# Kernel optimization log

Measured on AMD Instinct MI355X. Metric: run time of the kernel, lower is better.

Reference implementation:

```python
import jax, jax.numpy as jnp
import numpy as np

N = 524288      # points per view
S = 256         # superpoint segments
SEG = N // S    # points per segment (2048 >= 30 -> no small segments)
C = 96          # backbone_out_channels
K = 30          # samples per segment (matching_max_pair//S = 32 >= 30 -> capped at 30)
NEG = 30        # negatives sampled per anchor row
T_SUP = 0.5     # SupConLoss temperature
EPS = 1e-7


def setup_inputs() -> dict:
    key = jax.random.key(0)
    ks = jax.random.split(key, 4)
    view1_feat = jax.random.normal(ks[0], (N, C), jnp.float32)
    view2_feat = jax.random.normal(ks[1], (N, C), jnp.float32)
    region = (jnp.arange(N, dtype=jnp.int32) // SEG).astype(jnp.int32)
    # evenly spaced K sample indices inside each contiguous segment
    off = jnp.linspace(0.0, SEG - 1, K).astype(jnp.int32)
    idx_samples = (jnp.arange(S, dtype=jnp.int32)[:, None] * SEG + off[None, :]).reshape(-1)
    bg_mask = (jnp.arange(S) % 4) == 0  # some background superpoints
    gq_w = jax.random.normal(ks[2], (C, C), jnp.float32) * 0.02
    gk_w = jax.random.normal(ks[3], (C, C), jnp.float32) * 0.02
    z = jnp.zeros((C,), jnp.float32)
    o = jnp.ones((C,), jnp.float32)
    return dict(view1_feat=view1_feat, view2_feat=view2_feat,
                gq_w=gq_w, gq_b=z, gq_gamma=o, gq_beta=z,
                gk_w=gk_w, gk_b=z, gk_gamma=o, gk_beta=z,
                view1_region=region, view2_region=region,
                idx_samples=idx_samples, bg_mask=bg_mask)


def _head(x, w, b, gamma, beta):
    # Linear -> BatchNorm1d (batch stats, training mode) -> ReLU
    y = x @ w.T + b
    mu = y.mean(axis=0)
    var = jnp.var(y, axis=0)
    y = (y - mu) * jax.lax.rsqrt(var + 1e-5) * gamma + beta
    return jax.nn.relu(y)


def _segment_mean(x, seg, n):
    s = jax.ops.segment_sum(x, seg, num_segments=n)
    cnt = jax.ops.segment_sum(jnp.ones((x.shape[0], 1), x.dtype), seg, num_segments=n)
    return s / jnp.maximum(cnt, 1.0)


def _l2norm(x):
    return x / (jnp.linalg.norm(x, axis=1, keepdims=True) + EPS)


def _supcon(sim, pos, neg):
    # SupConLoss(temperature=0.5, scale_by_temperature=False, is_positive_in_denom=True)
    logits = sim / T_SUP
    denom_mask = pos | neg
    neg_inf = jnp.finfo(logits.dtype).min
    lse = jax.scipy.special.logsumexp(jnp.where(denom_mask, logits, neg_inf), axis=1)
    log_prob = logits - lse[:, None]
    row = jnp.sum(jnp.where(pos, log_prob, 0.0), axis=1) / jnp.sum(pos, axis=1).astype(logits.dtype)
    return -jnp.mean(row)


def reference(view1_feat, view2_feat, gq_w, gq_b, gq_gamma, gq_beta,
              gk_w, gk_b, gk_gamma, gk_beta,
              view1_region, view2_region, idx_samples, bg_mask):
    Sk = S * K
    rows = jnp.arange(S)[:, None]

    # ---- Lcon: raw-feature superpoint anchors vs sampled points ----
    anchor = _l2norm(_segment_mean(view2_feat, view2_region, S))          # [S, C]
    samples = _l2norm(view1_feat[idx_samples])                            # [S*K, C]
    sim = anchor @ samples.T                                              # [S, S*K]

    col_seg = jnp.arange(Sk) // K
    pos1 = rows == col_seg[None, :]                                       # block-diagonal positives

    # 30 evenly spaced negatives among the Sk-K non-positive columns per row
    M = Sk - K
    p = jnp.linspace(0.0, M - 1, NEG).astype(jnp.int32)                   # [NEG]
    actual = jnp.where(p[None, :] < rows * K, p[None, :], p[None, :] + K) # skip own block
    neg1 = jnp.zeros((S, Sk), bool).at[jnp.broadcast_to(rows, (S, NEG)), actual].set(True)
    Lcon = _supcon(sim, pos1, neg1)

    # ---- Lcon_2: projected (g_q / g_k head) features, top-k positives, background-split negatives ----
    v2g = _head(view2_feat, gq_w, gq_b, gq_gamma, gq_beta)
    v1g = _head(view1_feat, gk_w, gk_b, gk_gamma, gk_beta)
    anchor2 = _l2norm(_segment_mean(v2g, view2_region, S))
    samples2 = _l2norm(v1g[idx_samples])
    sim2 = anchor2 @ samples2.T                                           # [S, S*K]

    _, tk = jax.lax.top_k(sim2, K)
    pos2 = jnp.zeros((S, Sk), bool).at[jnp.broadcast_to(rows, (S, K)), tk].set(True)

    bg_col = jnp.repeat(bg_mask, K)                                       # [S*K]
    neg2 = jnp.where(bg_mask[:, None], ~bg_col[None, :], bg_col[None, :]) & (~pos1)
    Lcon2 = _supcon(sim2, pos2, neg2)

    return Lcon + Lcon2


if __name__ == '__main__':
    out = reference(**setup_inputs())
    print(out)
```

## Files before the change

### kernel.cpp

```cpp
#include <hip/hip_runtime.h>
#include <math.h>

#define SK 7680
#define NPTS 524288

#define WS_GQ_PART  0
#define WS_GK_PART  6144
#define WS_GQ_SCALE 12288
#define WS_GQ_SHIFT 12384
#define WS_GK_SCALE 12480
#define WS_GK_SHIFT 12576
#define WS_SEGX2    21888
#define WS_SEGG2    46464
#define WS_ANCHOR1  71040
#define WS_ANCHOR2  95616
#define WS_SAMPT    120192
#define WS_SAMP2T   857472
#define WS_SROW     1594752
#define WS_ZERO_CNT 71040

typedef __attribute__((ext_vector_type(8))) short bf16x8;
typedef __attribute__((ext_vector_type(4))) float f32x4;

#define AS1 __attribute__((address_space(1)))
#define AS3 __attribute__((address_space(3)))

__device__ __forceinline__ void gl16(const float* g, char* l){
  __builtin_amdgcn_global_load_lds((const AS1 unsigned*)g, (AS3 unsigned*)l, 16, 0, 0);
}

__device__ __forceinline__ bf16x8 pack8(float4 a, float4 b){
  union { unsigned u[4]; bf16x8 v; } r;
  asm("v_cvt_pk_bf16_f32 %0, %1, %2" : "=v"(r.u[0]) : "v"(a.x), "v"(a.y));
  asm("v_cvt_pk_bf16_f32 %0, %1, %2" : "=v"(r.u[1]) : "v"(a.z), "v"(a.w));
  asm("v_cvt_pk_bf16_f32 %0, %1, %2" : "=v"(r.u[2]) : "v"(b.x), "v"(b.y));
  asm("v_cvt_pk_bf16_f32 %0, %1, %2" : "=v"(r.u[3]) : "v"(b.z), "v"(b.w));
  return r.v;
}
__device__ __forceinline__ bf16x8 pack8v(f32x4 a, f32x4 b){
  union { unsigned u[4]; bf16x8 v; } r;
  asm("v_cvt_pk_bf16_f32 %0, %1, %2" : "=v"(r.u[0]) : "v"(a[0]), "v"(a[1]));
  asm("v_cvt_pk_bf16_f32 %0, %1, %2" : "=v"(r.u[1]) : "v"(a[2]), "v"(a[3]));
  asm("v_cvt_pk_bf16_f32 %0, %1, %2" : "=v"(r.u[2]) : "v"(b[0]), "v"(b[1]));
  asm("v_cvt_pk_bf16_f32 %0, %1, %2" : "=v"(r.u[3]) : "v"(b[2]), "v"(b[3]));
  return r.v;
}
__device__ __forceinline__ float4 ld4(const float* p){
  return *reinterpret_cast<const float4*>(p);
}

__device__ __forceinline__ void build_wf(const float* __restrict__ W, bf16x8 wf[3][3],
                                         int oh, int lr, int g){
  #pragma unroll
  for (int i=0;i<3;i++){
    const float* wr = W + (unsigned)((oh*3+i)*16+lr)*96 + g*8;
    #pragma unroll
    for (int kt=0;kt<3;kt++)
      wf[i][kt] = pack8(ld4(wr + kt*32), ld4(wr + kt*32 + 4));
  }
}

#define VMC_WAIT(it)                                                   \
  if ((it) <= 4)      { asm volatile("s_waitcnt vmcnt(9)" ::: "memory"); } \
  else if ((it) == 5) { asm volatile("s_waitcnt vmcnt(6)" ::: "memory"); } \
  else if ((it) == 6) { asm volatile("s_waitcnt vmcnt(3)" ::: "memory"); } \
  else                { asm volatile("s_waitcnt vmcnt(0)" ::: "memory"); }

__global__ __launch_bounds__(256) void stats_both(
    const float* __restrict__ V1, const float* __restrict__ V2,
    const float* __restrict__ Wk, const float* __restrict__ Wq,
    float* __restrict__ gpartK, float* __restrict__ gpartQ)
{
  __shared__ __align__(16) float xtile[4][3072];
  __shared__ float red[96];
  __shared__ float red2[96];
  const int tid = threadIdx.x;
  const int l = tid & 63, w = tid >> 6;
  const int g = l >> 4, lr = l & 15;
  const int rg = w & 1, oh = w >> 1;
  const int R = rg*16 + lr;

  const int r_ = blockIdx.x & 15;
  const int g_ = blockIdx.x >> 4;
  const bool isv2 = (r_ >= 8);
  const int  sub  = (r_ & 7) * 256 + g_;
  const float* X = isv2 ? V2 : V1;
  const float* W = isv2 ? Wq : Wk;

  bf16x8 wf[3][3];
  build_wf(W, wf, oh, lr, g);
  if (tid < 96){ red[tid]=0.f; red2[tid]=0.f; }

  int so[3];
  #pragma unroll
  for (int i=0;i<3;i++){
    int s = i*256 + tid;
    int r = s/24, cp = s%24;
    int c = (cp & ~7) | ((cp & 7) ^ (r & 7));
    so[i] = r*96 + c*4;
  }
  const float* base = X + (long)sub*24576;
  char* lbase_c = (char*)&xtile[0][0] + w*1024;

  unsigned lb = (unsigned)(uintptr_t)&xtile[0][0];
  const unsigned a0base = lb + R*384 + (unsigned)((( 2*g   ) ^ (R&7))*16);
  const unsigned a1base = lb + R*384 + (unsigned)((((2*g)|1) ^ (R&7))*16);

#define STAGE(t) {                                        \
    const float* tb = base + (t)*3072;                    \
    char* ld = lbase_c + ((t)&3)*12288;                   \
    gl16(tb + so[0], ld);                                 \
    gl16(tb + so[1], ld + 4096);                          \
    gl16(tb + so[2], ld + 8192); }

  STAGE(0) STAGE(1) STAGE(2) STAGE(3)

  float sY[3]={0.f,0.f,0.f}, sY2[3]={0.f,0.f,0.f};

  #pragma unroll 1
  for (int it=0; it<8; ++it){
    VMC_WAIT(it)
    __builtin_amdgcn_s_barrier();
    const unsigned boff = (unsigned)(it&3)*12288u;
    unsigned addrA = a0base + boff, addrB = a1base + boff;
    f32x4 xA0,xA1,xA2,xB0,xB1,xB2;
    asm volatile(
      "ds_read_b128 %0, %6\n\t"
      "ds_read_b128 %1, %6 offset:128\n\t"
      "ds_read_b128 %2, %6 offset:256\n\t"
      "ds_read_b128 %3, %7\n\t"
      "ds_read_b128 %4, %7 offset:128\n\t"
      "ds_read_b128 %5, %7 offset:256\n\t"
      "s_waitcnt lgkmcnt(0)"
      : "=&v"(xA0),"=&v"(xA1),"=&v"(xA2),"=&v"(xB0),"=&v"(xB1),"=&v"(xB2)
      : "v"(addrA), "v"(addrB) : "memory");
    __builtin_amdgcn_sched_barrier(0);
    __builtin_amdgcn_s_barrier();
    if (it<4) STAGE(it+4)
    bf16x8 a0 = pack8v(xA0,xB0), a1 = pack8v(xA1,xB1), a2 = pack8v(xA2,xB2);
    #pragma unroll
    for (int i=0;i<3;i++){
      f32x4 acc = {0.f,0.f,0.f,0.f};
      acc = __builtin_amdgcn_mfma_f32_16x16x32_bf16(a0, wf[i][0], acc, 0,0,0);
      acc = __builtin_amdgcn_mfma_f32_16x16x32_bf16(a1, wf[i][1], acc, 0,0,0);
      acc = __builtin_amdgcn_mfma_f32_16x16x32_bf16(a2, wf[i][2], acc, 0,0,0);
      sY[i]  += acc[0]+acc[1]+acc[2]+acc[3];
      sY2[i]  = fmaf(acc[0],acc[0],fmaf(acc[1],acc[1],
                fmaf(acc[2],acc[2],fmaf(acc[3],acc[3],sY2[i]))));
    }
  }
#undef STAGE

  __syncthreads();
  #pragma unroll
  for (int i=0;i<3;i++){
    float s = sY[i], s2 = sY2[i];
    s  += __shfl_xor(s,16);  s  += __shfl_xor(s,32);
    s2 += __shfl_xor(s2,16); s2 += __shfl_xor(s2,32);
    if (g==0){
      atomicAdd(&red[(oh*3+i)*16+lr],  s);
      atomicAdd(&red2[(oh*3+i)*16+lr], s2);
    }
  }
  __syncthreads();
  if (tid<96){
    float* dst = (isv2 ? gpartQ : gpartK) + (sub & 31)*192;
    atomicAdd(dst+tid,    red[tid]);
    atomicAdd(dst+96+tid, red2[tid]);
  }
}

__global__ __launch_bounds__(256) void head_apply_mfma(
    const float* __restrict__ X, const float* __restrict__ W,
    const float* __restrict__ scale, const float* __restrict__ shift,
    float* __restrict__ gsegRaw, float* __restrict__ gsegBN)
{
  __shared__ __align__(16) float xtile[4][3072];
  __shared__ float red[96];
  __shared__ float rsg[96];
  const int tid = threadIdx.x;
  const int l = tid & 63, w = tid >> 6;
  const int g = l >> 4, lr = l & 15;
  const int rg = w & 1, oh = w >> 1;
  const int R = rg*16 + lr;

  const int sub = ((blockIdx.x & 7) << 8) | (blockIdx.x >> 3);

  bf16x8 wf[3][3];
  build_wf(W, wf, oh, lr, g);
  if (tid < 96){ red[tid]=0.f; rsg[tid]=0.f; }

  float sc[3], sh[3];
  #pragma unroll
  for (int i=0;i<3;i++){
    sc[i]=scale[(oh*3+i)*16+lr]; sh[i]=shift[(oh*3+i)*16+lr];
  }

  int so[3], ck[3];
  #pragma unroll
  for (int i=0;i<3;i++){
    int s = i*256 + tid;
    int r = s/24, cp = s%24;
    int c = (cp & ~7) | ((cp & 7) ^ (r & 7));
    so[i] = r*96 + c*4;
    ck[i] = c;
  }
  const float* base = X + (long)sub*24576;
  char* lbase_c = (char*)&xtile[0][0] + w*1024;

  unsigned lb = (unsigned)(uintptr_t)&xtile[0][0];
  const unsigned a0base = lb + R*384 + (unsigned)((( 2*g   ) ^ (R&7))*16);
  const unsigned a1base = lb + R*384 + (unsigned)((((2*g)|1) ^ (R&7))*16);
  const unsigned acbase = lb + tid*16;

#define STAGE(t) {                                        \
    const float* tb = base + (t)*3072;                    \
    char* ld = lbase_c + ((t)&3)*12288;                   \
    gl16(tb + so[0], ld);                                 \
    gl16(tb + so[1], ld + 4096);                          \
    gl16(tb + so[2], ld + 8192); }

  STAGE(0) STAGE(1) STAGE(2) STAGE(3)

  float zs[3]={0.f,0.f,0.f};
  f32x4 cs0={0.f,0.f,0.f,0.f}, cs1={0.f,0.f,0.f,0.f}, cs2={0.f,0.f,0.f,0.f};

  #pragma unroll 1
  for (int it=0; it<8; ++it){
    VMC_WAIT(it)
    __builtin_amdgcn_s_barrier();
    const unsigned boff = (unsigned)(it&3)*12288u;
    unsigned addrA = a0base + boff, addrB = a1base + boff, addrC = acbase + boff;
    f32x4 xA0,xA1,xA2,xB0,xB1,xB2,xC0,xC1,xC2;
    asm volatile(
      "ds_read_b128 %0, %9\n\t"
      "ds_read_b128 %1, %9 offset:128\n\t"
      "ds_read_b128 %2, %9 offset:256\n\t"
      "ds_read_b128 %3, %10\n\t"
      "ds_read_b128 %4, %10 offset:128\n\t"
      "ds_read_b128 %5, %10 offset:256\n\t"
      "ds_read_b128 %6, %11\n\t"
      "ds_read_b128 %7, %11 offset:4096\n\t"
      "ds_read_b128 %8, %11 offset:8192\n\t"
      "s_waitcnt lgkmcnt(0)"
      : "=&v"(xA0),"=&v"(xA1),"=&v"(xA2),"=&v"(xB0),"=&v"(xB1),"=&v"(xB2),
        "=&v"(xC0),"=&v"(xC1),"=&v"(xC2)
      : "v"(addrA), "v"(addrB), "v"(addrC) : "memory");
    __builtin_amdgcn_sched_barrier(0);
    __builtin_amdgcn_s_barrier();
    if (it<4) STAGE(it+4)
    cs0[0]+=xC0[0]; cs0[1]+=xC0[1]; cs0[2]+=xC0[2]; cs0[3]+=xC0[3];
    cs1[0]+=xC1[0]; cs1[1]+=xC1[1]; cs1[2]+=xC1[2]; cs1[3]+=xC1[3];
    cs2[0]+=xC2[0]; cs2[1]+=xC2[1]; cs2[2]+=xC2[2]; cs2[3]+=xC2[3];
    bf16x8 a0 = pack8v(xA0,xB0), a1 = pack8v(xA1,xB1), a2 = pack8v(xA2,xB2);
    #pragma unroll
    for (int i=0;i<3;i++){
      f32x4 acc = {0.f,0.f,0.f,0.f};
      acc = __builtin_amdgcn_mfma_f32_16x16x32_bf16(a0, wf[i][0], acc, 0,0,0);
      acc = __builtin_amdgcn_mfma_f32_16x16x32_bf16(a1, wf[i][1], acc, 0,0,0);
      acc = __builtin_amdgcn_mfma_f32_16x16x32_bf16(a2, wf[i][2], acc, 0,0,0);
      zs[i] += fmaxf(fmaf(acc[0],sc[i],sh[i]),0.f)
             + fmaxf(fmaf(acc[1],sc[i],sh[i]),0.f)
             + fmaxf(fmaf(acc[2],sc[i],sh[i]),0.f)
             + fmaxf(fmaf(acc[3],sc[i],sh[i]),0.f);
    }
  }
#undef STAGE

  __syncthreads();
  #pragma unroll
  for (int k=0;k<4;k++) atomicAdd(&rsg[ck[0]*4+k], cs0[k]);
  #pragma unroll
  for (int k=0;k<4;k++) atomicAdd(&rsg[ck[1]*4+k], cs1[k]);
  #pragma unroll
  for (int k=0;k<4;k++) atomicAdd(&rsg[ck[2]*4+k], cs2[k]);
  #pragma unroll
  for (int i=0;i<3;i++){
    float s = zs[i];
    s += __shfl_xor(s,16); s += __shfl_xor(s,32);
    if (g==0) atomicAdd(&red[(oh*3+i)*16+lr], s);
  }
  __syncthreads();
  if (tid<96){
    atomicAdd(gsegRaw + (sub>>3)*96 + tid, rsg[tid]);
    atomicAdd(gsegBN  + (sub>>3)*96 + tid, red[tid]);
  }
}

__global__ void bn_params_kernel(const float* __restrict__ gq_gamma, const float* __restrict__ gq_beta,
                                 const float* __restrict__ gk_gamma, const float* __restrict__ gk_beta,
                                 float* __restrict__ ws)
{
  const int t = threadIdx.x;
  const float invN = 1.0f/(float)NPTS;
  if (t < 96){
    float s=0.f, s2=0.f;
    #pragma unroll 4
    for (int p=0;p<32;p++){
      s  += ws[WS_GQ_PART + p*192 + t];
      s2 += ws[WS_GQ_PART + p*192 + 96 + t];
    }
    float mu  = s*invN;
    float var = s2*invN - mu*mu;
    float sc  = gq_gamma[t]*rsqrtf(var + 1e-5f);
    ws[WS_GQ_SCALE+t] = sc;
    ws[WS_GQ_SHIFT+t] = gq_beta[t] - mu*sc;
  } else if (t < 192){
    int c = t-96;
    float s=0.f, s2=0.f;
    #pragma unroll 4
    for (int p=0;p<32;p++){
      s  += ws[WS_GK_PART + p*192 + c];
      s2 += ws[WS_GK_PART + p*192 + 96 + c];
    }
    float mu  = s*invN;
    float var = s2*invN - mu*mu;
    float sc  = gk_gamma[c]*rsqrtf(var + 1e-5f);
    ws[WS_GK_SCALE+c] = sc;
    ws[WS_GK_SHIFT+c] = gk_beta[c] - mu*sc;
  }
}

__global__ __launch_bounds__(128) void anchor2x_kernel(
    const float* __restrict__ seg1, float* __restrict__ dst1,
    const float* __restrict__ seg2, float* __restrict__ dst2)
{
  __shared__ float red[128];
  const int t = threadIdx.x, s = blockIdx.x & 255;
  const float* segsum = (blockIdx.x < 256) ? seg1 : seg2;
  float* dst          = (blockIdx.x < 256) ? dst1 : dst2;
  float m = 0.f;
  if (t<96) m = segsum[s*96+t] * (1.0f/2048.0f);
  red[t] = m*m;
  __syncthreads();
  for (int off=64; off>0; off>>=1){
    if (t<off) red[t]+=red[t+off];
    __syncthreads();
  }
  float inv = 1.0f/(sqrtf(red[0]) + 1e-7f);
  if (t<96) dst[s*96+t] = m*inv;
}

__device__ __forceinline__ void fma_row(float4& acc, const float4 x,
    const float4 w0, const float4 w1, const float4 w2, const float4 w3){
  acc.x = fmaf(x.x,w0.x, fmaf(x.y,w1.x, fmaf(x.z,w2.x, fmaf(x.w,w3.x, acc.x))));
  acc.y = fmaf(x.x,w0.y, fmaf(x.y,w1.y, fmaf(x.z,w2.y, fmaf(x.w,w3.y, acc.y))));
  acc.z = fmaf(x.x,w0.z, fmaf(x.y,w1.z, fmaf(x.z,w2.z, fmaf(x.w,w3.z, acc.z))));
  acc.w = fmaf(x.x,w0.w, fmaf(x.y,w1.w, fmaf(x.z,w2.w, fmaf(x.w,w3.w, acc.w))));
}
__device__ __forceinline__ void load_W(const float* __restrict__ W, float* Ws, int tid){
  #pragma unroll
  for (int i=0;i<12;i++){
    int f = i*768 + tid*4;
    int oc = f/96, k = f%96;
    float4 w4 = *reinterpret_cast<const float4*>(W + f);
    Ws[(k+0)*100+oc]=w4.x; Ws[(k+1)*100+oc]=w4.y;
    Ws[(k+2)*100+oc]=w4.z; Ws[(k+3)*100+oc]=w4.w;
  }
}
__device__ __forceinline__ void gemm_tile(const float* Xs, const float* Ws,
    int ocg, int rowg, int r0, float4 acc[4]){
  const float4* Xs4 = reinterpret_cast<const float4*>(Xs);
  const float4* Ws4 = reinterpret_cast<const float4*>(Ws);
  acc[0]=acc[1]=acc[2]=acc[3]=make_float4(0.f,0.f,0.f,0.f);
  #pragma unroll 4
  for (int k4=0;k4<24;k4++){
    float4 w0 = Ws4[(k4*4+0)*25 + ocg];
    float4 w1 = Ws4[(k4*4+1)*25 + ocg];
    float4 w2 = Ws4[(k4*4+2)*25 + ocg];
    float4 w3 = Ws4[(k4*4+3)*25 + ocg];
    #pragma unroll
    for (int jj=0;jj<4;jj++){
      float4 xv = Xs4[(r0+jj)*25 + (k4 ^ rowg)];
      fma_row(acc[jj], xv, w0, w1, w2, w3);
    }
  }
}

__global__ __launch_bounds__(192) void samples_kernel(
    const float* __restrict__ V1, const float* __restrict__ W,
    const float* __restrict__ scale, const float* __restrict__ shift,
    const int* __restrict__ idxs,
    float* __restrict__ sampT, float* __restrict__ samp2T)
{
  __shared__ __align__(16) float Ws[9600];
  __shared__ __align__(16) float Xs[3200];
  __shared__ __align__(16) float Gs[3200];
  __shared__ float invr[32], invh[32];
  const int tid = threadIdx.x;
  const int ocg = tid % 24, rowg = tid / 24;
  const int oc0 = ocg*4,  r0  = rowg*4;
  load_W(W, Ws, tid);
  const int base = blockIdx.x * 32;
  #pragma unroll
  for (int i=0;i<4;i++){
    int f = i*768 + tid*4;
    int row = f/96, col = f%96;
    int g = idxs[base+row];
    float4 v = *reinterpret_cast<const float4*>(V1 + g*96 + col);
    *reinterpret_cast<float4*>(Xs + row*100 + (col ^ ((row>>2)<<2))) = v;
  }
  __syncthreads();
  if (tid<32){
    float s=0.f;
    #pragma unroll
    for (int k=0;k<96;k++){ float v=Xs[tid*100+(k^((tid>>2)<<2))]; s=fmaf(v,v,s); }
    invr[tid]=1.0f/(sqrtf(s)+1e-7f);
  }
  __syncthreads();
  {
    int rr=tid&31, kg=tid>>5;
    float inv=invr[rr];
    #pragma unroll
    for (int kk=0;kk<16;kk++){
      int k=kg*16+kk;
      sampT[(long)(base+rr)*96 + k] = Xs[rr*100 + (k ^ ((rr>>2)<<2))]*inv;
    }
  }
  float4 acc[4];
  gemm_tile(Xs, Ws, ocg, rowg, r0, acc);
  float4 sc = make_float4(scale[oc0],scale[oc0+1],scale[oc0+2],scale[oc0+3]);
  float4 sh = make_float4(shift[oc0],shift[oc0+1],shift[oc0+2],shift[oc0+3]);
  #pragma unroll
  for (int jj=0;jj<4;jj++){
    int rr=r0+jj;
    float4 g;
    g.x=fmaxf(fmaf(acc[jj].x,sc.x,sh.x),0.f);
    g.y=fmaxf(fmaf(acc[jj].y,sc.y,sh.y),0.f);
    g.z=fmaxf(fmaf(acc[jj].z,sc.z,sh.z),0.f);
    g.w=fmaxf(fmaf(acc[jj].w,sc.w,sh.w),0.f);
    *reinterpret_cast<float4*>(Gs + rr*100 + (oc0 ^ ((rr>>2)<<2))) = g;
  }
  __syncthreads();
  if (tid<32){
    float s=0.f;
    #pragma unroll
    for (int k=0;k<96;k++){ float v=Gs[tid*100+(k^((tid>>2)<<2))]; s=fmaf(v,v,s); }
    invh[tid]=1.0f/(sqrtf(s)+1e-7f);
  }
  __syncthreads();
  {
    int rr=tid&31, kg=tid>>5;
    float inv=invh[rr];
    #pragma unroll
    for (int kk=0;kk<16;kk++){
      int k=kg*16+kk;
      samp2T[(long)(base+rr)*96 + k] = Gs[rr*100 + (k ^ ((rr>>2)<<2))]*inv;
    }
  }
}

__global__ __launch_bounds__(256) void sim2_mfma(
    const float* __restrict__ anchor2, const float* __restrict__ samp2,
    float* __restrict__ srowG)
{
  const int tid = threadIdx.x;
  const int l = tid & 63, w = tid >> 6;
  const int g = l >> 4, lr = l & 15;
  const int rowbase = blockIdx.y * 16;
  const int colbase = blockIdx.x * 256 + w * 64;

  bf16x8 af[3];
  const float* ar = anchor2 + (rowbase + lr)*96 + g*8;
  #pragma unroll
  for (int kt=0; kt<3; ++kt)
    af[kt] = pack8(ld4(ar + kt*32), ld4(ar + kt*32 + 4));

  #pragma unroll
  for (int sub=0; sub<4; ++sub){
    const float* br = samp2 + (long)(colbase + sub*16 + lr)*96 + g*8;
    float4 b00 = ld4(br);    float4 b01 = ld4(br+4);
    float4 b10 = ld4(br+32); float4 b11 = ld4(br+36);
    float4 b20 = ld4(br+64); float4 b21 = ld4(br+68);
    f32x4 acc = {0.f,0.f,0.f,0.f};
    acc = __builtin_amdgcn_mfma_f32_16x16x32_bf16(af[0], pack8(b00,b01), acc, 0,0,0);
    acc = __builtin_amdgcn_mfma_f32_16x16x32_bf16(af[1], pack8(b10,b11), acc, 0,0,0);
    acc = __builtin_amdgcn_mfma_f32_16x16x32_bf16(af[2], pack8(b20,b21), acc, 0,0,0);
    const int col  = colbase + sub*16 + lr;
    const int row0 = rowbase + g*4;
    #pragma unroll
    for (int i=0;i<4;i++)
      srowG[(long)(row0+i)*SK + col] = acc[i];
  }
}

__global__ __launch_bounds__(256) void lcon12_kernel(
    const float* __restrict__ anchor1, const float* __restrict__ sampT,
    const float* __restrict__ srowG, const int* __restrict__ bg,
    float* __restrict__ out)
{
  const int tid = threadIdx.x;
  if (blockIdx.x >= 256){
    __shared__ float a[96];
    const int r = blockIdx.x - 256;
    if (tid < 64){
      for (int i=tid;i<96;i+=64) a[i]=anchor1[r*96+i];
      int c = 0;
      if (tid<30) c = r*30+tid;
      else if (tid<60){
        int j = tid-30;
        int p = (int)((double)j * 7649.0 / 29.0);
        c = (p < r*30) ? p : p+30;
      }
      float s=0.f;
      if (tid<60){
        const float* sr = sampT + (long)c*96;
        #pragma unroll
        for (int k4=0;k4<24;k4++){
          float4 v = *reinterpret_cast<const float4*>(sr + k4*4);
          s = fmaf(a[k4*4+0],v.x, fmaf(a[k4*4+1],v.y,
              fmaf(a[k4*4+2],v.z, fmaf(a[k4*4+3],v.w, s))));
        }
      }
      float logit = 2.0f*s;
      float se = (tid<60) ? expf(logit) : 0.f;
      float sp = (tid<30) ? logit : 0.f;
      #pragma unroll
      for (int off=32; off; off>>=1){ se += __shfl_xor(se,off); sp += __shfl_xor(sp,off); }
      if (tid==0){
        float row = sp*(1.0f/30.0f) - logf(se);
        atomicAdd(out, -row*(1.0f/256.0f));
      }
    }
    return;
  }
  __shared__ float wvv[4];
  __shared__ int   wcc[4];
  __shared__ int   winc_s;
  __shared__ int   sel[30];
  const int r = blockIdx.x;
  const int lane = tid & 63, wid = tid >> 6;
  const float* __restrict__ rowp = srowG + (long)r*SK;
  float val[30];
  #pragma unroll
  for (int j=0;j<30;j++) val[j] = rowp[(j<<8) + tid];
  unsigned mask=0; float possum=0.f;
  for (int it=0; it<30; ++it){
    float bv = -3.0e38f; int bc = 1<<30;
    #pragma unroll
    for (int j=0;j<30;j++){
      if (!((mask>>j)&1u)){
        float v = val[j]; int c = tid + (j<<8);
        if (v > bv || (v == bv && c < bc)){ bv=v; bc=c; }
      }
    }
    #pragma unroll
    for (int off=32; off; off>>=1){
      float ov = __shfl_xor(bv, off); int ocx = __shfl_xor(bc, off);
      if (ov > bv || (ov == bv && ocx < bc)){ bv=ov; bc=ocx; }
    }
    if (lane==0){ wvv[wid]=bv; wcc[wid]=bc; }
    __syncthreads();
    if (tid==0){
      float v=wvv[0]; int c=wcc[0];
      #pragma unroll
      for (int w2=1;w2<4;w2++){
        if (wvv[w2]>v || (wvv[w2]==v && wcc[w2]<c)){ v=wvv[w2]; c=wcc[w2]; }
      }
      winc_s=c; sel[it]=c; possum += v;
    }
    __syncthreads();
    int c = winc_s;
    if ((c & 255) == tid) mask |= 1u << (c >> 8);
  }
  const int bgr = bg[r];
  float se=0.f;
  #pragma unroll
  for (int j=0;j<30;j++){
    int c = tid + (j<<8);
    int seg = c/30;
    int bgc = bg[seg];
    bool nf = ((bgr!=0) ? (bgc==0) : (bgc!=0)) && (seg != r);
    if (nf) se += expf(2.0f*val[j]);
  }
  #pragma unroll
  for (int off=32; off; off>>=1) se += __shfl_xor(se, off);
  if (lane==0) wvv[wid]=se;
  __syncthreads();
  float ex=0.f;
  if (tid<30){
    int c = sel[tid]; int seg=c/30; int bgc=bg[seg];
    bool nf = ((bgr!=0) ? (bgc==0) : (bgc!=0)) && (seg != r);
    if (!nf) ex = expf(2.0f*rowp[c]);
  }
  if (wid==0){
    #pragma unroll
    for (int off=32; off; off>>=1) ex += __shfl_xor(ex, off);
  }
  if (tid==0){
    float lse = logf(wvv[0]+wvv[1]+wvv[2]+wvv[3] + ex);
    float row = possum*(2.0f/30.0f) - lse;
    atomicAdd(out, -row*(1.0f/256.0f));
  }
}

extern "C" void kernel_launch(void* const* d_in, const int* in_sizes, int n_in,
                              void* d_out, int out_size, void* d_ws, size_t ws_size,
                              hipStream_t stream) {
  (void)in_sizes; (void)n_in; (void)out_size; (void)ws_size;
  const float* v1       = (const float*)d_in[0];
  const float* v2       = (const float*)d_in[1];
  const float* gq_w     = (const float*)d_in[2];
  const float* gq_gamma = (const float*)d_in[4];
  const float* gq_beta  = (const float*)d_in[5];
  const float* gk_w     = (const float*)d_in[6];
  const float* gk_gamma = (const float*)d_in[8];
  const float* gk_beta  = (const float*)d_in[9];
  const int*   idxs     = (const int*)d_in[12];
  const int*   bg       = (const int*)d_in[13];
  float* ws  = (float*)d_ws;
  float* out = (float*)d_out;

  hipMemsetAsync(ws, 0, (size_t)WS_ZERO_CNT*sizeof(float), stream);
  hipMemsetAsync(out, 0, sizeof(float), stream);

  stats_both<<<4096,256,0,stream>>>(v1, v2, gk_w, gq_w, ws+WS_GK_PART, ws+WS_GQ_PART);
  bn_params_kernel<<<1,192,0,stream>>>(gq_gamma, gq_beta, gk_gamma, gk_beta, ws);
  samples_kernel<<<240,192,0,stream>>>(v1, gk_w, ws+WS_GK_SCALE, ws+WS_GK_SHIFT, idxs,
                                       ws+WS_SAMPT, ws+WS_SAMP2T);
  head_apply_mfma<<<2048,256,0,stream>>>(v2, gq_w, ws+WS_GQ_SCALE, ws+WS_GQ_SHIFT,
                                         ws+WS_SEGX2, ws+WS_SEGG2);
  anchor2x_kernel<<<512,128,0,stream>>>(ws+WS_SEGX2, ws+WS_ANCHOR1, ws+WS_SEGG2, ws+WS_ANCHOR2);
  sim2_mfma<<<dim3(30,16),256,0,stream>>>(ws+WS_ANCHOR2, ws+WS_SAMP2T, ws+WS_SROW);
  lcon12_kernel<<<512,256,0,stream>>>(ws+WS_ANCHOR1, ws+WS_SAMPT, ws+WS_SROW, bg, out);
}
```

Before: 264.4 us.

## Cache view2 as bf16 in stats pass and reread it in head apply

Result: slower. 316.0 us (+19.5%).

```diff
diff --git a/kernel.cpp b/kernel.cpp
--- a/kernel.cpp
+++ b/kernel.cpp
@@ -17,6 +17,7 @@
 #define WS_SAMPT    120192
 #define WS_SAMP2T   857472
 #define WS_SROW     1594752
+#define WS_XB       3560832
 #define WS_ZERO_CNT 71040
 
 typedef __attribute__((ext_vector_type(8))) short bf16x8;
@@ -26,6 +27,9 @@
 #define AS3 __attribute__((address_space(3)))
 
 __device__ __forceinline__ void gl16(const float* g, char* l){
+  __builtin_amdgcn_global_load_lds((const AS1 unsigned*)g, (AS3 unsigned*)l, 16, 0, 0);
+}
+__device__ __forceinline__ void gl16b(const char* g, char* l){
   __builtin_amdgcn_global_load_lds((const AS1 unsigned*)g, (AS3 unsigned*)l, 16, 0, 0);
 }
 
@@ -48,6 +52,9 @@
 __device__ __forceinline__ float4 ld4(const float* p){
   return *reinterpret_cast<const float4*>(p);
 }
+__device__ __forceinline__ uint4 asu4(bf16x8 a){
+  union { bf16x8 v; uint4 u; } c; c.v = a; return c.u;
+}
 
 __device__ __forceinline__ void build_wf(const float* __restrict__ W, bf16x8 wf[3][3],
                                          int oh, int lr, int g){
@@ -65,15 +72,26 @@
   else if ((it) == 5) { asm volatile("s_waitcnt vmcnt(6)" ::: "memory"); } \
   else if ((it) == 6) { asm volatile("s_waitcnt vmcnt(3)" ::: "memory"); } \
   else                { asm volatile("s_waitcnt vmcnt(0)" ::: "memory"); }
+#define VMC_WAIT_S(it)                                                 \
+  if ((it)==0)      { asm volatile("s_waitcnt vmcnt(9)"  ::: "memory"); } \
+  else if ((it)==1) { asm volatile("s_waitcnt vmcnt(12)" ::: "memory"); } \
+  else if ((it)==2) { asm volatile("s_waitcnt vmcnt(15)" ::: "memory"); } \
+  else if ((it)==3) { asm volatile("s_waitcnt vmcnt(18)" ::: "memory"); } \
+  else if ((it)==4) { asm volatile("s_waitcnt vmcnt(21)" ::: "memory"); } \
+  else if ((it)==5) { asm volatile("s_waitcnt vmcnt(18)" ::: "memory"); } \
+  else if ((it)==6) { asm volatile("s_waitcnt vmcnt(15)" ::: "memory"); } \
+  else              { asm volatile("s_waitcnt vmcnt(12)" ::: "memory"); }
 
 __global__ __launch_bounds__(256) void stats_both(
     const float* __restrict__ V1, const float* __restrict__ V2,
     const float* __restrict__ Wk, const float* __restrict__ Wq,
-    float* __restrict__ gpartK, float* __restrict__ gpartQ)
+    float* __restrict__ gpartK, float* __restrict__ gpartQ,
+    float* __restrict__ gseg, char* __restrict__ xb)
 {
   __shared__ __align__(16) float xtile[4][3072];
   __shared__ float red[96];
   __shared__ float red2[96];
+  __shared__ float rsg[96];
   const int tid = threadIdx.x;
   const int l = tid & 63, w = tid >> 6;
   const int g = l >> 4, lr = l & 15;
@@ -86,10 +104,11 @@
   const int  sub  = (r_ & 7) * 256 + g_;
   const float* X = isv2 ? V2 : V1;
   const float* W = isv2 ? Wq : Wk;
+  const bool store_wave = isv2 && (oh == 0);
 
   bf16x8 wf[3][3];
   build_wf(W, wf, oh, lr, g);
-  if (tid < 96){ red[tid]=0.f; red2[tid]=0.f; }
+  if (tid < 96){ red[tid]=0.f; red2[tid]=0.f; rsg[tid]=0.f; }
 
   int so[3];
   #pragma unroll
@@ -105,6 +124,9 @@
   unsigned lb = (unsigned)(uintptr_t)&xtile[0][0];
   const unsigned a0base = lb + R*384 + (unsigned)((( 2*g   ) ^ (R&7))*16);
   const unsigned a1base = lb + R*384 + (unsigned)((((2*g)|1) ^ (R&7))*16);
+
+  const int qchunk = (g ^ ((R>>1)&3)) ^ (R&3);
+  char* xb_ptr = xb + (size_t)(sub*256 + R)*192 + (size_t)qchunk*16;
 
 #define STAGE(t) {                                        \
     const float* tb = base + (t)*3072;                    \
@@ -116,10 +138,12 @@
   STAGE(0) STAGE(1) STAGE(2) STAGE(3)
 
   float sY[3]={0.f,0.f,0.f}, sY2[3]={0.f,0.f,0.f};
+  f32x4 csA0={0,0,0,0}, csA1={0,0,0,0}, csA2={0,0,0,0};
+  f32x4 csB0={0,0,0,0}, csB1={0,0,0,0}, csB2={0,0,0,0};
 
   #pragma unroll 1
   for (int it=0; it<8; ++it){
-    VMC_WAIT(it)
+    if (store_wave){ VMC_WAIT_S(it) } else { VMC_WAIT(it) }
     __builtin_amdgcn_s_barrier();
     const unsigned boff = (unsigned)(it&3)*12288u;
     unsigned addrA = a0base + boff, addrB = a1base + boff;
@@ -136,8 +160,20 @@
       : "v"(addrA), "v"(addrB) : "memory");
     __builtin_amdgcn_sched_barrier(0);
     __builtin_amdgcn_s_barrier();
+    bf16x8 a0 = pack8v(xA0,xB0), a1 = pack8v(xA1,xB1), a2 = pack8v(xA2,xB2);
     if (it<4) STAGE(it+4)
-    bf16x8 a0 = pack8v(xA0,xB0), a1 = pack8v(xA1,xB1), a2 = pack8v(xA2,xB2);
+    if (store_wave){
+      csA0[0]+=xA0[0]; csA0[1]+=xA0[1]; csA0[2]+=xA0[2]; csA0[3]+=xA0[3];
+      csA1[0]+=xA1[0]; csA1[1]+=xA1[1]; csA1[2]+=xA1[2]; csA1[3]+=xA1[3];
+      csA2[0]+=xA2[0]; csA2[1]+=xA2[1]; csA2[2]+=xA2[2]; csA2[3]+=xA2[3];
+      csB0[0]+=xB0[0]; csB0[1]+=xB0[1]; csB0[2]+=xB0[2]; csB0[3]+=xB0[3];
+      csB1[0]+=xB1[0]; csB1[1]+=xB1[1]; csB1[2]+=xB1[2]; csB1[3]+=xB1[3];
+      csB2[0]+=xB2[0]; csB2[1]+=xB2[1]; csB2[2]+=xB2[2]; csB2[3]+=xB2[3];
+      uint4* xp = reinterpret_cast<uint4*>(xb_ptr + it*6144);
+      xp[0] = asu4(a0);
+      xp[4] = asu4(a1);
+      xp[8] = asu4(a2);
+    }
     #pragma unroll
     for (int i=0;i<3;i++){
       f32x4 acc = {0.f,0.f,0.f,0.f};
@@ -162,33 +198,43 @@
       atomicAdd(&red2[(oh*3+i)*16+lr], s2);
     }
   }
+  if (store_wave){
+    const int cA = 2*g, cB = 2*g+1;
+    #pragma unroll
+    for (int k=0;k<4;k++){
+      atomicAdd(&rsg[cA*4+k],      csA0[k]);
+      atomicAdd(&rsg[(cA+8)*4+k],  csA1[k]);
+      atomicAdd(&rsg[(cA+16)*4+k], csA2[k]);
+      atomicAdd(&rsg[cB*4+k],      csB0[k]);
+      atomicAdd(&rsg[(cB+8)*4+k],  csB1[k]);
+      atomicAdd(&rsg[(cB+16)*4+k], csB2[k]);
+    }
+  }
   __syncthreads();
   if (tid<96){
     float* dst = (isv2 ? gpartQ : gpartK) + (sub & 31)*192;
     atomicAdd(dst+tid,    red[tid]);
     atomicAdd(dst+96+tid, red2[tid]);
-  }
-}
-
-__global__ __launch_bounds__(256) void head_apply_mfma(
-    const float* __restrict__ X, const float* __restrict__ W,
+    if (isv2) atomicAdd(gseg + (sub>>3)*96 + tid, rsg[tid]);
+  }
+}
+
+__global__ __launch_bounds__(256) void head_apply_bf16(
+    const char* __restrict__ xb, const float* __restrict__ W,
     const float* __restrict__ scale, const float* __restrict__ shift,
-    float* __restrict__ gsegRaw, float* __restrict__ gsegBN)
+    float* __restrict__ gsegBN)
 {
-  __shared__ __align__(16) float xtile[4][3072];
+  __shared__ __align__(16) char xt[2][12288];
   __shared__ float red[96];
-  __shared__ float rsg[96];
   const int tid = threadIdx.x;
   const int l = tid & 63, w = tid >> 6;
   const int g = l >> 4, lr = l & 15;
   const int rg = w & 1, oh = w >> 1;
-  const int R = rg*16 + lr;
-
-  const int sub = ((blockIdx.x & 7) << 8) | (blockIdx.x >> 3);
+  const int Rr = rg*16 + lr;
 
   bf16x8 wf[3][3];
   build_wf(W, wf, oh, lr, g);
-  if (tid < 96){ red[tid]=0.f; rsg[tid]=0.f; }
+  if (tid < 96) red[tid]=0.f;
 
   float sc[3], sh[3];
   #pragma unroll
@@ -196,84 +242,71 @@
     sc[i]=scale[(oh*3+i)*16+lr]; sh[i]=shift[(oh*3+i)*16+lr];
   }
 
-  int so[3], ck[3];
-  #pragma unroll
-  for (int i=0;i<3;i++){
-    int s = i*256 + tid;
-    int r = s/24, cp = s%24;
-    int c = (cp & ~7) | ((cp & 7) ^ (r & 7));
-    so[i] = r*96 + c*4;
-    ck[i] = c;
-  }
-  const float* base = X + (long)sub*24576;
-  char* lbase_c = (char*)&xtile[0][0] + w*1024;
-
-  unsigned lb = (unsigned)(uintptr_t)&xtile[0][0];
-  const unsigned a0base = lb + R*384 + (unsigned)((( 2*g   ) ^ (R&7))*16);
-  const unsigned a1base = lb + R*384 + (unsigned)((((2*g)|1) ^ (R&7))*16);
-  const unsigned acbase = lb + tid*16;
+  const char* base = xb + (size_t)blockIdx.x*4*12288;
+  char* lbase = &xt[0][0] + w*1024;
+  unsigned lb = (unsigned)(uintptr_t)&xt[0][0];
+  const unsigned q0 = (unsigned)((g ^ ((Rr>>1)&3)) ^ (Rr&3));
+  const unsigned afb0 = lb + (unsigned)(Rr*192) + q0*16u;
+  const unsigned afb1 = afb0 + 32u*192u;
 
 #define STAGE(t) {                                        \
-    const float* tb = base + (t)*3072;                    \
-    char* ld = lbase_c + ((t)&3)*12288;                   \
-    gl16(tb + so[0], ld);                                 \
-    gl16(tb + so[1], ld + 4096);                          \
-    gl16(tb + so[2], ld + 8192); }
-
-  STAGE(0) STAGE(1) STAGE(2) STAGE(3)
+    const char* tb = base + (t)*12288;                    \
+    char* ld = lbase + ((t)&1)*12288;                     \
+    gl16b(tb + tid*16,        ld);                        \
+    gl16b(tb + 4096 + tid*16, ld + 4096);                 \
+    gl16b(tb + 8192 + tid*16, ld + 8192); }
+
+  STAGE(0) STAGE(1)
 
   float zs[3]={0.f,0.f,0.f};
-  f32x4 cs0={0.f,0.f,0.f,0.f}, cs1={0.f,0.f,0.f,0.f}, cs2={0.f,0.f,0.f,0.f};
 
   #pragma unroll 1
-  for (int it=0; it<8; ++it){
-    VMC_WAIT(it)
+  for (int t=0; t<4; ++t){
+    if (t<3){ asm volatile("s_waitcnt vmcnt(3)" ::: "memory"); }
+    else    { asm volatile("s_waitcnt vmcnt(0)" ::: "memory"); }
     __builtin_amdgcn_s_barrier();
-    const unsigned boff = (unsigned)(it&3)*12288u;
-    unsigned addrA = a0base + boff, addrB = a1base + boff, addrC = acbase + boff;
-    f32x4 xA0,xA1,xA2,xB0,xB1,xB2,xC0,xC1,xC2;
+    const unsigned boff = (unsigned)(t&1)*12288u;
+    unsigned aS0 = afb0 + boff, aS1 = afb1 + boff;
+    bf16x8 f00,f01,f02,f10,f11,f12;
     asm volatile(
-      "ds_read_b128 %0, %9\n\t"
-      "ds_read_b128 %1, %9 offset:128\n\t"
-      "ds_read_b128 %2, %9 offset:256\n\t"
-      "ds_read_b128 %3, %10\n\t"
-      "ds_read_b128 %4, %10 offset:128\n\t"
-      "ds_read_b128 %5, %10 offset:256\n\t"
-      "ds_read_b128 %6, %11\n\t"
-      "ds_read_b128 %7, %11 offset:4096\n\t"
-      "ds_read_b128 %8, %11 offset:8192\n\t"
+      "ds_read_b128 %0, %6\n\t"
+      "ds_read_b128 %1, %6 offset:64\n\t"
+      "ds_read_b128 %2, %6 offset:128\n\t"
+      "ds_read_b128 %3, %7\n\t"
+      "ds_read_b128 %4, %7 offset:64\n\t"
+      "ds_read_b128 %5, %7 offset:128\n\t"
       "s_waitcnt lgkmcnt(0)"
-      : "=&v"(xA0),"=&v"(xA1),"=&v"(xA2),"=&v"(xB0),"=&v"(xB1),"=&v"(xB2),
-        "=&v"(xC0),"=&v"(xC1),"=&v"(xC2)
-      : "v"(addrA), "v"(addrB), "v"(addrC) : "memory");
+      : "=&v"(f00),"=&v"(f01),"=&v"(f02),"=&v"(f10),"=&v"(f11),"=&v"(f12)
+      : "v"(aS0), "v"(aS1) : "memory");
     __builtin_amdgcn_sched_barrier(0);
     __builtin_amdgcn_s_barrier();
-    if (it<4) STAGE(it+4)
-    cs0[0]+=xC0[0]; cs0[1]+=xC0[1]; cs0[2]+=xC0[2]; cs0[3]+=xC0[3];
-    cs1[0]+=xC1[0]; cs1[1]+=xC1[1]; cs1[2]+=xC1[2]; cs1[3]+=xC1[3];
-    cs2[0]+=xC2[0]; cs2[1]+=xC2[1]; cs2[2]+=xC2[2]; cs2[3]+=xC2[3];
-    bf16x8 a0 = pack8v(xA0,xB0), a1 = pack8v(xA1,xB1), a2 = pack8v(xA2,xB2);
+    if (t<2) STAGE(t+2)
     #pragma unroll
     for (int i=0;i<3;i++){
       f32x4 acc = {0.f,0.f,0.f,0.f};
-      acc = __builtin_amdgcn_mfma_f32_16x16x32_bf16(a0, wf[i][0], acc, 0,0,0);
-      acc = __builtin_amdgcn_mfma_f32_16x16x32_bf16(a1, wf[i][1], acc, 0,0,0);
-      acc = __builtin_amdgcn_mfma_f32_16x16x32_bf16(a2, wf[i][2], acc, 0,0,0);
+      acc = __builtin_amdgcn_mfma_f32_16x16x32_bf16(f00, wf[i][0], acc, 0,0,0);
+      acc = __builtin_amdgcn_mfma_f32_16x16x32_bf16(f01, wf[i][1], acc, 0,0,0);
+      acc = __builtin_amdgcn_mfma_f32_16x16x32_bf16(f02, wf[i][2], acc, 0,0,0);
       zs[i] += fmaxf(fmaf(acc[0],sc[i],sh[i]),0.f)
              + fmaxf(fmaf(acc[1],sc[i],sh[i]),0.f)
              + fmaxf(fmaf(acc[2],sc[i],sh[i]),0.f)
              + fmaxf(fmaf(acc[3],sc[i],sh[i]),0.f);
     }
+    #pragma unroll
+    for (int i=0;i<3;i++){
+      f32x4 acc = {0.f,0.f,0.f,0.f};
+      acc = __builtin_amdgcn_mfma_f32_16x16x32_bf16(f10, wf[i][0], acc, 0,0,0);
+      acc = __builtin_amdgcn_mfma_f32_16x16x32_bf16(f11, wf[i][1], acc, 0,0,0);
+      acc = __builtin_amdgcn_mfma_f32_16x16x32_bf16(f12, wf[i][2], acc, 0,0,0);
+      zs[i] += fmaxf(fmaf(acc[0],sc[i],sh[i]),0.f)
+             + fmaxf(fmaf(acc[1],sc[i],sh[i]),0.f)
+             + fmaxf(fmaf(acc[2],sc[i],sh[i]),0.f)
+             + fmaxf(fmaf(acc[3],sc[i],sh[i]),0.f);
+    }
   }
 #undef STAGE
 
   __syncthreads();
-  #pragma unroll
-  for (int k=0;k<4;k++) atomicAdd(&rsg[ck[0]*4+k], cs0[k]);
-  #pragma unroll
-  for (int k=0;k<4;k++) atomicAdd(&rsg[ck[1]*4+k], cs1[k]);
-  #pragma unroll
-  for (int k=0;k<4;k++) atomicAdd(&rsg[ck[2]*4+k], cs2[k]);
   #pragma unroll
   for (int i=0;i<3;i++){
     float s = zs[i];
@@ -281,10 +314,7 @@
     if (g==0) atomicAdd(&red[(oh*3+i)*16+lr], s);
   }
   __syncthreads();
-  if (tid<96){
-    atomicAdd(gsegRaw + (sub>>3)*96 + tid, rsg[tid]);
-    atomicAdd(gsegBN  + (sub>>3)*96 + tid, red[tid]);
-  }
+  if (tid<96) atomicAdd(gsegBN + (blockIdx.x>>3)*96 + tid, red[tid]);
 }
 
 __global__ void bn_params_kernel(const float* __restrict__ gq_gamma, const float* __restrict__ gq_beta,
@@ -610,16 +640,17 @@
   const int*   bg       = (const int*)d_in[13];
   float* ws  = (float*)d_ws;
   float* out = (float*)d_out;
-
-  hipMemsetAsync(ws, 0, (size_t)WS_ZERO_CNT*sizeof(float), stream);
-  hipMemsetAsync(out, 0, sizeof(float), stream);
-
-  stats_both<<<4096,256,0,stream>>>(v1, v2, gk_w, gq_w, ws+WS_GK_PART, ws+WS_GQ_PART);
+  char*  xb  = (char*)(ws + WS_XB);
+
+  (void)hipMemsetAsync(ws, 0, (size_t)WS_ZERO_CNT*sizeof(float), stream);
+  (void)hipMemsetAsync(out, 0, sizeof(float), stream);
+
+  stats_both<<<4096,256,0,stream>>>(v1, v2, gk_w, gq_w,
+                                    ws+WS_GK_PART, ws+WS_GQ_PART, ws+WS_SEGX2, xb);
   bn_params_kernel<<<1,192,0,stream>>>(gq_gamma, gq_beta, gk_gamma, gk_beta, ws);
   samples_kernel<<<240,192,0,stream>>>(v1, gk_w, ws+WS_GK_SCALE, ws+WS_GK_SHIFT, idxs,
                                        ws+WS_SAMPT, ws+WS_SAMP2T);
-  head_apply_mfma<<<2048,256,0,stream>>>(v2, gq_w, ws+WS_GQ_SCALE, ws+WS_GQ_SHIFT,
-                                         ws+WS_SEGX2, ws+WS_SEGG2);
+  head_apply_bf16<<<2048,256,0,stream>>>(xb, gq_w, ws+WS_GQ_SCALE, ws+WS_GQ_SHIFT, ws+WS_SEGG2);
   anchor2x_kernel<<<512,128,0,stream>>>(ws+WS_SEGX2, ws+WS_ANCHOR1, ws+WS_SEGG2, ws+WS_ANCHOR2);
   sim2_mfma<<<dim3(30,16),256,0,stream>>>(ws+WS_ANCHOR2, ws+WS_SAMP2T, ws+WS_SROW);
   lcon12_kernel<<<512,256,0,stream>>>(ws+WS_ANCHOR1, ws+WS_SAMPT, ws+WS_SROW, bg, out);
```
